# Performance work log

Measured on AMD Instinct MI355X. Metric: run time of the kernel, lower is better.

The kernel has to match this reference:

```python
import math
import jax, jax.numpy as jnp
import numpy as np

L, F, K = 3, 128, 20          # layers, hidden size, rbf size
CUTOFF = 5.0
B, NPER, EPER = 4, 4096, 49152  # graphs, nodes/graph, edges/graph
NVOC = 119                    # len(ase.data.atomic_numbers)
PNAMES = ['atom_emb','pot_W','pot_b','init_W1','init_b1','init_W2','init_b2','vec_w',
          'filt_W','filt_b','msg_W1','msg_b1','msg_W2','msg_b2','U_W','V_W',
          'upd_W1','upd_b1','upd_W2','upd_b2']


def _painn(atom_xyz, cell, nodes, atom_edges, edges_displacement, V_flat, E_flat, p):
    N = B * NPER
    pos = atom_xyz.reshape(N, 3)
    # edge_offset = cumsum(num_nodes) ; all graphs have NPER nodes
    off = (jnp.arange(B, dtype=atom_edges.dtype) * NPER)[:, None, None]
    edges = (atom_edges + off).reshape(B * EPER, 2)
    # calc_distance with periodic cell offsets
    disp = jnp.einsum('bec,bcd->bed', edges_displacement, cell).reshape(B * EPER, 3)
    send, recv = edges[:, 0], edges[:, 1]
    diff = pos[recv] - (pos[send] + disp)                       # [E,3]
    dist = jnp.sqrt(jnp.sum(diff * diff, axis=1, keepdims=True))  # [E,1]
    # sinc RBF expansion
    n_range = jnp.arange(1, K + 1, dtype=jnp.float32)
    edge_state = jnp.sin(dist * n_range * (math.pi / CUTOFF)) / dist  # [E,K]
    # init scalar features: Embedding(Z) || Linear(V) -> MLP
    s_atom = p['atom_emb'][nodes.reshape(N)]                    # [N,F]
    s_pot = V_flat @ p['pot_W'].T + p['pot_b']                  # [N,F]
    h = jnp.concatenate([s_atom, s_pot], axis=-1)
    s = jax.nn.silu(h @ p['init_W1'].T + p['init_b1']) @ p['init_W2'].T + p['init_b2']  # [N,F]
    # init vector features: no-bias Linear(1->F) on E field
    v = E_flat[:, :, None] * p['vec_w']                         # [N,3,F]
    cut = jnp.where(dist < CUTOFF, 0.5 * (jnp.cos(math.pi * dist / CUTOFF) + 1.0), 0.0)  # [E,1]
    dirn = diff / jnp.maximum(dist, 1e-12)                      # [E,3]
    s_list, v_list = [], []
    for l in range(L):
        # --- PaiNNInteraction ---
        fw = (edge_state @ p['filt_W'][l].T + p['filt_b'][l]) * cut                # [E,3F]
        so = jax.nn.silu(s @ p['msg_W1'][l].T + p['msg_b1'][l]) @ p['msg_W2'][l].T + p['msg_b2'][l]  # [N,3F]
        fo = fw * so[send]                                                          # [E,3F]
        g_sv, g_ev, g_ns = jnp.split(fo, 3, axis=1)
        msg_s = s[send] * g_ns                                                      # [E,F]
        msg_v = v[send] * g_sv[:, None, :] + g_ev[:, None, :] * dirn[:, :, None]    # [E,3,F]
        s = s + jax.ops.segment_sum(msg_s, recv, num_segments=N)
        v = v + jax.ops.segment_sum(msg_v, recv, num_segments=N)
        # --- PaiNNUpdate ---
        Uv = v @ p['U_W'][l].T                                                      # [N,3,F]
        Vv = v @ p['V_W'][l].T                                                      # [N,3,F]
        Vn = jnp.sqrt(jnp.sum(Vv * Vv, axis=1))                                     # [N,F]
        m = jnp.concatenate([s, Vn], axis=1)
        m = jax.nn.silu(m @ p['upd_W1'][l].T + p['upd_b1'][l]) @ p['upd_W2'][l].T + p['upd_b2'][l]
        a_ss, a_sv, a_vv = jnp.split(m, 3, axis=1)
        s = s + a_ss + a_sv * jnp.sum(Uv * Vv, axis=1)
        v = v + a_vv[:, None, :] * Uv
        s_list.append(s)
        v_list.append(v)
    # pack trajectory: [L,N,1,F] scalar || [L,N,3,F] vector -> [L,N,4,F]
    return jnp.concatenate([jnp.stack(s_list)[:, :, None, :], jnp.stack(v_list)], axis=2)


def setup_inputs() -> dict:
    key = jax.random.key(0)
    ks = iter(jax.random.split(key, 48))
    def nrm(shape, scale=0.05):
        return jax.random.normal(next(ks), shape, dtype=jnp.float32) * scale
    atom_xyz = jax.random.uniform(next(ks), (B, NPER, 3), dtype=jnp.float32) * 30.0
    cell = jnp.tile(jnp.eye(3, dtype=jnp.float32)[None] * 30.0, (B, 1, 1))
    nodes = jax.random.randint(next(ks), (B, NPER), 0, NVOC)
    e0 = jax.random.randint(next(ks), (B, EPER), 0, NPER)
    delta = jax.random.randint(next(ks), (B, EPER), 1, NPER)
    e1 = (e0 + delta) % NPER  # sender != receiver -> no zero-distance edges
    atom_edges = jnp.stack([e0, e1], axis=-1)
    edges_displacement = jax.random.randint(next(ks), (B, EPER, 3), -1, 2).astype(jnp.float32)
    V_flat = nrm((B * NPER, 1), 1.0)
    E_flat = nrm((B * NPER, 3), 1.0)
    params = dict(
        atom_emb=nrm((NVOC, F), 1.0),
        pot_W=nrm((F, 1)), pot_b=nrm((F,)),
        init_W1=nrm((F, 2 * F)), init_b1=nrm((F,)),
        init_W2=nrm((F, F)), init_b2=nrm((F,)),
        vec_w=nrm((F,)),
        filt_W=nrm((L, 3 * F, K)), filt_b=nrm((L, 3 * F)),
        msg_W1=nrm((L, F, F)), msg_b1=nrm((L, F)),
        msg_W2=nrm((L, 3 * F, F)), msg_b2=nrm((L, 3 * F)),
        U_W=nrm((L, F, F)), V_W=nrm((L, F, F)),
        upd_W1=nrm((L, F, 2 * F)), upd_b1=nrm((L, F)),
        upd_W2=nrm((L, 3 * F, F)), upd_b2=nrm((L, 3 * F)),
    )
    return dict(atom_xyz=atom_xyz, cell=cell, nodes=nodes, atom_edges=atom_edges,
                edges_displacement=edges_displacement, V_flat=V_flat, E_flat=E_flat, **params)


def reference(atom_xyz, cell, nodes, atom_edges, edges_displacement, V_flat, E_flat,
              atom_emb, pot_W, pot_b, init_W1, init_b1, init_W2, init_b2, vec_w,
              filt_W, filt_b, msg_W1, msg_b1, msg_W2, msg_b2, U_W, V_W,
              upd_W1, upd_b1, upd_W2, upd_b2):
    p = dict(zip(PNAMES, (atom_emb, pot_W, pot_b, init_W1, init_b1, init_W2, init_b2, vec_w,
                          filt_W, filt_b, msg_W1, msg_b1, msg_W2, msg_b2, U_W, V_W,
                          upd_W1, upd_b1, upd_W2, upd_b2)))
    return _painn(atom_xyz, cell, nodes, atom_edges, edges_displacement, V_flat, E_flat, p)
```

## Files before the change

kernel.cpp:

```cpp
#include <hip/hip_runtime.h>
#include <math.h>

#define NPER  4096
#define NTOT  16384
#define EPER  49152
#define ETOT  196608
#define FD    128
#define F3    384
#define KR    20
#define PI_F  3.14159265358979f

typedef unsigned short u16;
typedef __attribute__((ext_vector_type(8))) short s16x8;
typedef __attribute__((ext_vector_type(4))) float f32x4;
typedef _Float16 h16x2 __attribute__((ext_vector_type(2)));
typedef _Float16 h16x4 __attribute__((ext_vector_type(4)));
typedef _Float16 h16x8 __attribute__((ext_vector_type(8)));

#if defined(__has_builtin)
#if __has_builtin(__builtin_amdgcn_fdot2)
#define FDOT2(a,b,c) __builtin_amdgcn_fdot2((a),(b),(c),false)
#endif
#endif
#ifndef FDOT2
#define FDOT2(a,b,c) ((float)(a)[0]*(float)(b)[0] + (float)(a)[1]*(float)(b)[1] + (c))
#endif

__device__ __forceinline__ float silu_f(float x){ return x / (1.0f + __expf(-x)); }
__device__ __forceinline__ u16 f2b(float x){
    unsigned u = __float_as_uint(x);
    u = u + 0x7FFFu + ((u >> 16) & 1u);
    return (u16)(u >> 16);
}
__device__ __forceinline__ float b2f(u16 h){ return __uint_as_float(((unsigned)h) << 16); }

struct __align__(16) EdgeRec {
    float4 ed;
    h16x8  es0;
    h16x8  es1;
    h16x4  es2;
    h16x4  pad;
};

__global__ __launch_bounds__(256) void edge_kernel(
    const float* __restrict__ xyz, const float* __restrict__ cell,
    const int* __restrict__ aedges, const float* __restrict__ edisp,
    int* __restrict__ sendb, int* __restrict__ recvb,
    EdgeRec* __restrict__ erec, int* __restrict__ counts)
{
    int e = blockIdx.x * blockDim.x + threadIdx.x;
    if (e >= ETOT) return;
    int b = e / EPER;
    int s = aedges[(size_t)e*2+0] + b*NPER;
    int r = aedges[(size_t)e*2+1] + b*NPER;
    const float* cb = cell + b*9;
    float c0 = edisp[(size_t)e*3+0], c1 = edisp[(size_t)e*3+1], c2 = edisp[(size_t)e*3+2];
    float diff[3];
    #pragma unroll
    for (int d=0; d<3; ++d) {
        float disp = c0*cb[d] + c1*cb[3+d] + c2*cb[6+d];
        diff[d] = xyz[(size_t)r*3+d] - (xyz[(size_t)s*3+d] + disp);
    }
    float dist = sqrtf(diff[0]*diff[0]+diff[1]*diff[1]+diff[2]*diff[2]);
    float cut = (dist < 5.0f) ? 0.5f*(__cosf(PI_F*dist*0.2f)+1.0f) : 0.0f;
    float invg = 1.0f/fmaxf(dist,1e-12f);
    EdgeRec rec;
    rec.ed = make_float4(diff[0]*invg, diff[1]*invg, diff[2]*invg, cut);
    float theta = dist*(PI_F*0.2f);
    float s1 = __sinf(theta), cth = __cosf(theta);
    float scale = cut / dist;
    float twoc = 2.f*cth;
    float sm1 = 0.f, sk = s1;
    _Float16 esv[20];
    #pragma unroll
    for (int k=0;k<20;++k){
        esv[k] = (_Float16)(sk*scale);
        float nx = twoc*sk - sm1;
        sm1 = sk; sk = nx;
    }
    union { h16x8 v; _Float16 h[8]; } u0, u1;
    union { h16x4 v; _Float16 h[4]; } u2;
    #pragma unroll
    for (int i=0;i<8;++i){ u0.h[i]=esv[i]; u1.h[i]=esv[8+i]; }
    #pragma unroll
    for (int i=0;i<4;++i) u2.h[i]=esv[16+i];
    rec.es0=u0.v; rec.es1=u1.v; rec.es2=u2.v;
    rec.pad = (h16x4)((_Float16)0);
    erec[e] = rec;
    sendb[e]=s; recvb[e]=r;
    atomicAdd(&counts[r],1);
}

__global__ __launch_bounds__(1024) void scan_kernel(const int* __restrict__ counts,
                                                    int* __restrict__ row_off)
{
    __shared__ int sdata[1024];
    int t = threadIdx.x;
    int base = t * 16;
    int local[16];
    int s = 0;
    #pragma unroll
    for (int i=0;i<16;++i){ local[i]=s; s += counts[base+i]; }
    sdata[t] = s;
    __syncthreads();
    for (int off=1; off<1024; off<<=1) {
        int val = (t>=off) ? sdata[t-off] : 0;
        __syncthreads();
        sdata[t] += val;
        __syncthreads();
    }
    int chunk_off = (t==0) ? 0 : sdata[t-1];
    #pragma unroll
    for (int i=0;i<16;++i) row_off[base+i] = chunk_off + local[i];
    if (t==1023) row_off[NTOT] = sdata[1023];
}

__global__ __launch_bounds__(256) void fill_kernel(
    const int* __restrict__ recvb, const int* __restrict__ sendb,
    const EdgeRec* __restrict__ erec,
    const int* __restrict__ row_off, int* __restrict__ cursor,
    int* __restrict__ sd_csr, EdgeRec* __restrict__ erec_csr)
{
    int e = blockIdx.x * blockDim.x + threadIdx.x;
    if (e >= ETOT) return;
    int r = recvb[e];
    int slot = atomicAdd(&cursor[r], 1);
    int pos = row_off[r] + slot;
    sd_csr[pos] = sendb[e];
    erec_csr[pos] = erec[e];
}

__global__ __launch_bounds__(256) void wconv_kernel(
    const float* __restrict__ w0, const float* __restrict__ w1,
    const float* __restrict__ w2, const float* __restrict__ w3,
    const float* __restrict__ w4, const float* __restrict__ w5,
    const float* __restrict__ w6, const float* __restrict__ w7,
    u16* __restrict__ dst)
{
    int t = blockIdx.x*256 + threadIdx.x;
    if (t >= 589824) return;
    const float* src; int off; int d = t;
    if      (t < 32768)  { src=w0; off=t; }
    else if (t < 49152)  { src=w1; off=t-32768; }
    else if (t < 98304)  { src=w2; off=t-49152; }
    else if (t < 245760) { src=w3; off=t-98304; }
    else if (t < 294912) { int o=t-245760; int l=o>>14; int r=o&16383; src=w4; off=o;
                           d = 245760 + l*32768 + r; }
    else if (t < 344064) { int o=t-294912; int l=o>>14; int r=o&16383; src=w5; off=o;
                           d = 245760 + l*32768 + 16384 + r; }
    else if (t < 442368) { src=w6; off=t-344064; }
    else                 { src=w7; off=t-442368; }
    dst[d] = f2b(src[off]);
}

__global__ __launch_bounds__(256) void wfilt_kernel(const float* __restrict__ fW,
                                                    _Float16* __restrict__ dst)
{
    int t = blockIdx.x*256 + threadIdx.x;
    if (t < 3*F3*KR) dst[t] = (_Float16)fW[t];
}

__global__ __launch_bounds__(256) void hbuild_kernel(const int* __restrict__ nodes,
    const float* __restrict__ atom_emb, const float* __restrict__ V_flat,
    const float* __restrict__ pot_W, const float* __restrict__ pot_b,
    u16* __restrict__ h)
{
    int t = blockIdx.x * blockDim.x + threadIdx.x;
    int n = t >> 8, k = t & 255;
    float val;
    if (k < FD) val = atom_emb[(size_t)nodes[n]*FD + k];
    else { int f = k - FD; val = V_flat[n]*pot_W[f] + pot_b[f]; }
    h[t] = f2b(val);
}

__global__ __launch_bounds__(256) void v0_kernel(const float* __restrict__ E_flat,
    const float* __restrict__ vec_w, float* __restrict__ v0, u16* __restrict__ vq)
{
    int t = blockIdx.x * blockDim.x + threadIdx.x;
    int n = t / F3, r = t - n*F3;
    int c = r >> 7, f = r & 127;
    float val = E_flat[(size_t)n*3 + c] * vec_w[f];
    v0[t] = val;
    vq[((size_t)n*FD + f)*4 + c] = f2b(val);
}

template<int ACT>
__global__ __launch_bounds__(256) void bgemm_kernel(
    const u16* __restrict__ A, int lda,
    const u16* __restrict__ W, int Kdim,
    const float* __restrict__ bias,
    float* __restrict__ C, int ldc,
    u16* __restrict__ Cb, int ldcb,
    u16* __restrict__ Cq, int qoff)
{
    const int tid  = threadIdx.x;
    const int wave = tid >> 6, lane = tid & 63;
    const int q = lane >> 4, im = lane & 15;
    const int row0 = blockIdx.y*64 + wave*16;
    const int col0 = blockIdx.x*64;
    f32x4 acc[4];
    #pragma unroll
    for (int n=0;n<4;++n) acc[n] = (f32x4){0.f,0.f,0.f,0.f};
    const u16* Ap = A + (size_t)(row0+im)*lda + q*8;
    const u16* Wp = W + (size_t)(col0+im)*Kdim + q*8;
    for (int k0 = 0; k0 < Kdim; k0 += 32) {
        s16x8 af = *(const s16x8*)(Ap + k0);
        #pragma unroll
        for (int n=0;n<4;++n) {
            s16x8 bf = *(const s16x8*)(Wp + (size_t)n*16*Kdim + k0);
            acc[n] = __builtin_amdgcn_mfma_f32_16x16x32_bf16(af, bf, acc[n], 0, 0, 0);
        }
    }
    #pragma unroll
    for (int n=0;n<4;++n) {
        int col = col0 + n*16 + im;
        float bv = bias ? bias[col] : 0.f;
        #pragma unroll
        for (int r=0;r<4;++r) {
            int row = row0 + q*4 + r;
            float v = acc[n][r] + bv;
            if (ACT) v = silu_f(v);
            if (C)  C[(size_t)row*ldc + col] = v;
            if (Cb) Cb[(size_t)row*ldcb + col] = f2b(v);
            if (Cq) Cq[((size_t)row*FD + (col & 127))*4 + (col >> 7) + qoff] = f2b(v);
        }
    }
}

#define HID_OFF(row, col2b) ((unsigned)((row)*256 + (col2b)*2) ^ ((unsigned)((row)&7) << 4))

__global__ __launch_bounds__(512) void msgmlp_kernel(
    const u16* __restrict__ A,
    const u16* __restrict__ W1,
    const float* __restrict__ b1,
    const u16* __restrict__ W2,
    const float* __restrict__ b2,
    u16* __restrict__ sq)
{
    __shared__ u16 hid[64*FD];
    const int tid = threadIdx.x;
    const int wave = tid >> 6, lane = tid & 63;
    const int q = lane >> 4, im = lane & 15;
    const int rw = (wave >> 1) * 16;
    const int ch = wave & 1;
    const int row0 = blockIdx.x * 64;
    {
        f32x4 acc[4];
        #pragma unroll
        for (int n=0;n<4;++n) acc[n] = (f32x4){0.f,0.f,0.f,0.f};
        const u16* Ap = A + (size_t)(row0+rw+im)*FD + q*8;
        #pragma unroll
        for (int k0=0;k0<FD;k0+=32) {
            s16x8 af = *(const s16x8*)(Ap + k0);
            #pragma unroll
            for (int n=0;n<4;++n) {
                s16x8 bf = *(const s16x8*)(W1 + (size_t)(ch*64+n*16+im)*FD + k0 + q*8);
                acc[n] = __builtin_amdgcn_mfma_f32_16x16x32_bf16(af, bf, acc[n], 0, 0, 0);
            }
        }
        #pragma unroll
        for (int n=0;n<4;++n) {
            int col = ch*64 + n*16 + im;
            float bv = b1[col];
            #pragma unroll
            for (int r=0;r<4;++r) {
                int row = rw + q*4 + r;
                *(u16*)((char*)hid + HID_OFF(row, col)) = f2b(silu_f(acc[n][r]+bv));
            }
        }
    }
    __syncthreads();
    s16x8 af[4];
    {
        int row = rw + im;
        #pragma unroll
        for (int k=0;k<4;++k)
            af[k] = *(const s16x8*)((char*)hid + HID_OFF(row, k*32+q*8));
    }
    #pragma unroll
    for (int jj=0;jj<4;++jj) {
        int j = ch*4 + jj;
        f32x4 a2[3];
        #pragma unroll
        for (int g=0;g<3;++g) a2[g] = (f32x4){0.f,0.f,0.f,0.f};
        #pragma unroll
        for (int k=0;k<4;++k) {
            #pragma unroll
            for (int g=0;g<3;++g) {
                s16x8 bf = *(const s16x8*)(W2 + (size_t)(g*128 + j*16 + im)*FD + k*32 + q*8);
                a2[g] = __builtin_amdgcn_mfma_f32_16x16x32_bf16(af[k], bf, a2[g], 0, 0, 0);
            }
        }
        int fcol = j*16 + im;
        float c0 = b2[fcol], c1 = b2[FD+fcol], c2 = b2[2*FD+fcol];
        #pragma unroll
        for (int r=0;r<4;++r) {
            int row = row0 + rw + q*4 + r;
            size_t t4 = ((size_t)row*FD + fcol)*4;
            unsigned pk = (unsigned)f2b(a2[0][r]+c0) | ((unsigned)f2b(a2[1][r]+c1) << 16);
            *(unsigned*)(sq + t4) = pk;
            sq[t4+2] = f2b(a2[2][r]+c2);
        }
    }
}

__global__ __launch_bounds__(512) void updmlp_kernel(
    const u16* __restrict__ A,
    const u16* __restrict__ W1,
    const float* __restrict__ b1,
    const u16* __restrict__ W2,
    const float* __restrict__ b2,
    const float* __restrict__ s_mid, const float* __restrict__ dotb,
    const float* __restrict__ v_mid, const float* __restrict__ Uv,
    float* __restrict__ outp, u16* __restrict__ s_bf,
    u16* __restrict__ sq, u16* __restrict__ vq)
{
    __shared__ u16 hid[64*FD];
    const int tid = threadIdx.x;
    const int wave = tid >> 6, lane = tid & 63;
    const int q = lane >> 4, im = lane & 15;
    const int rw = (wave >> 1) * 16;
    const int ch = wave & 1;
    const int row0 = blockIdx.x * 64;
    {
        f32x4 acc[4];
        #pragma unroll
        for (int n=0;n<4;++n) acc[n] = (f32x4){0.f,0.f,0.f,0.f};
        const u16* Ap = A + (size_t)(row0+rw+im)*256 + q*8;
        #pragma unroll
        for (int k0=0;k0<256;k0+=32) {
            s16x8 af = *(const s16x8*)(Ap + k0);
            #pragma unroll
            for (int n=0;n<4;++n) {
                s16x8 bf = *(const s16x8*)(W1 + (size_t)(ch*64+n*16+im)*256 + k0 + q*8);
                acc[n] = __builtin_amdgcn_mfma_f32_16x16x32_bf16(af, bf, acc[n], 0, 0, 0);
            }
        }
        #pragma unroll
        for (int n=0;n<4;++n) {
            int col = ch*64 + n*16 + im;
            float bv = b1[col];
            #pragma unroll
            for (int r=0;r<4;++r) {
                int row = rw + q*4 + r;
                *(u16*)((char*)hid + HID_OFF(row, col)) = f2b(silu_f(acc[n][r]+bv));
            }
        }
    }
    __syncthreads();
    s16x8 af[4];
    {
        int row = rw + im;
        #pragma unroll
        for (int k=0;k<4;++k)
            af[k] = *(const s16x8*)((char*)hid + HID_OFF(row, k*32+q*8));
    }
    #pragma unroll
    for (int jj=0;jj<4;++jj) {
        int j = ch*4 + jj;
        f32x4 a2[3];
        #pragma unroll
        for (int g=0;g<3;++g) a2[g] = (f32x4){0.f,0.f,0.f,0.f};
        #pragma unroll
        for (int k=0;k<4;++k) {
            #pragma unroll
            for (int g=0;g<3;++g) {
                s16x8 bf = *(const s16x8*)(W2 + (size_t)(g*128 + j*16 + im)*FD + k*32 + q*8);
                a2[g] = __builtin_amdgcn_mfma_f32_16x16x32_bf16(af[k], bf, a2[g], 0, 0, 0);
            }
        }
        int fcol = j*16 + im;
        float b_ss = b2[fcol], b_sv = b2[FD+fcol], b_vv = b2[2*FD+fcol];
        #pragma unroll
        for (int r=0;r<4;++r) {
            int row = row0 + rw + q*4 + r;
            float a_ss = a2[0][r] + b_ss;
            float a_sv = a2[1][r] + b_sv;
            float a_vv = a2[2][r] + b_vv;
            size_t t = (size_t)row*FD + fcol;
            float sval = s_mid[t] + a_ss + a_sv*dotb[t];
            outp[(size_t)row*512 + fcol] = sval;
            s_bf[t] = f2b(sval);
            sq[t*4 + 3] = f2b(sval);
            ushort4 pack;
            #pragma unroll
            for (int c=0;c<3;++c) {
                size_t vi = ((size_t)row*3 + c)*FD + fcol;
                float vval = v_mid[vi] + a_vv*Uv[((size_t)row*4 + c)*FD + fcol];
                outp[(size_t)row*512 + (1+c)*FD + fcol] = vval;
                ((u16*)&pack)[c] = f2b(vval);
            }
            ((u16*)&pack)[3] = 0;
            *(ushort4*)(vq + t*4) = pack;
        }
    }
}

__global__ __launch_bounds__(256) void uvdot_kernel(
    const u16* __restrict__ A,
    const u16* __restrict__ W,
    float* __restrict__ Uv,
    float* __restrict__ dotb,
    u16* __restrict__ mbuf)
{
    const int tid  = threadIdx.x;
    const int wave = tid >> 6, lane = tid & 63;
    const int q = lane >> 4, im = lane & 15;
    const int row0 = blockIdx.x*64 + wave*16;
    const int node = (row0 >> 2) + q;
    const u16* Ap = A + (size_t)(row0+im)*FD + q*8;
    s16x8 af[4];
    #pragma unroll
    for (int k=0;k<4;++k) af[k] = *(const s16x8*)(Ap + k*32);
    #pragma unroll
    for (int j=0;j<8;++j) {
        f32x4 aU = (f32x4){0.f,0.f,0.f,0.f};
        f32x4 aV = (f32x4){0.f,0.f,0.f,0.f};
        const u16* WpU = W + (size_t)(j*16+im)*FD + q*8;
        const u16* WpV = WpU + (size_t)128*FD;
        #pragma unroll
        for (int k=0;k<4;++k) {
            s16x8 bU = *(const s16x8*)(WpU + k*32);
            s16x8 bV = *(const s16x8*)(WpV + k*32);
            aU = __builtin_amdgcn_mfma_f32_16x16x32_bf16(af[k], bU, aU, 0, 0, 0);
            aV = __builtin_amdgcn_mfma_f32_16x16x32_bf16(af[k], bV, aV, 0, 0, 0);
        }
        int fcol = j*16 + im;
        float u0=aU[0], u1=aU[1], u2=aU[2];
        float w0=aV[0], w1=aV[1], w2=aV[2];
        dotb[(size_t)node*FD + fcol] = u0*w0 + u1*w1 + u2*w2;
        mbuf[(size_t)node*256 + FD + fcol] = f2b(sqrtf(w0*w0 + w1*w1 + w2*w2));
        size_t ub = ((size_t)node*4)*FD + fcol;
        Uv[ub]      = u0;
        Uv[ub+FD]   = u1;
        Uv[ub+2*FD] = u2;
    }
}

__device__ __forceinline__ void edge_step(
    const EdgeRec& er, ushort4 s4, ushort4 v4,
    const h16x2* wp,
    float b0, float b1, float b2,
    float& acc_s, float& av0, float& av1, float& av2)
{
    union { h16x8 v; h16x2 p[4]; } e0, e1;
    union { h16x4 v; h16x2 p[2]; } e2;
    e0.v = er.es0; e1.v = er.es1; e2.v = er.es2;
    h16x2 ep[10] = {e0.p[0],e0.p[1],e0.p[2],e0.p[3],
                    e1.p[0],e1.p[1],e1.p[2],e1.p[3],
                    e2.p[0],e2.p[1]};
    float4 ed = er.ed;
    float d0=0.f, d1=0.f, d2=0.f;
    #pragma unroll
    for (int j=0;j<10;++j){
        d0 = FDOT2(ep[j], wp[j],    d0);
        d1 = FDOT2(ep[j], wp[10+j], d1);
        d2 = FDOT2(ep[j], wp[20+j], d2);
    }
    float g_sv = d0 + b0*ed.w;
    float g_ev = d1 + b1*ed.w;
    float g_ns = d2 + b2*ed.w;
    float fo_sv = g_sv * b2f(s4.x);
    float fo_ev = g_ev * b2f(s4.y);
    float fo_ns = g_ns * b2f(s4.z);
    acc_s += b2f(s4.w) * fo_ns;
    av0 += b2f(v4.x)*fo_sv + fo_ev*ed.x;
    av1 += b2f(v4.y)*fo_sv + fo_ev*ed.y;
    av2 += b2f(v4.z)*fo_sv + fo_ev*ed.z;
}

__global__ __launch_bounds__(256) __attribute__((amdgpu_waves_per_eu(4,8)))
void agg_kernel(
    const float* __restrict__ s_prev_f, int s_ldaf,
    const float* __restrict__ v_prev_f, int v_nstrf,
    const ushort4* __restrict__ sq, const ushort4* __restrict__ vq,
    const EdgeRec* __restrict__ erec_csr,
    const int* __restrict__ sd_csr, const int* __restrict__ row_off,
    const _Float16* __restrict__ wf, const float* __restrict__ fb,
    float* __restrict__ s_mid, float* __restrict__ v_mid,
    u16* __restrict__ vmid4_bf, u16* __restrict__ mbuf)
{
    const int f   = threadIdx.x & 127;
    const int sub = threadIdx.x >> 7;
    h16x2 wp[30];
    #pragma unroll
    for (int rsel=0; rsel<3; ++rsel){
        const h16x4* rp = (const h16x4*)(wf + (size_t)(rsel*FD + f)*KR);
        #pragma unroll
        for (int i=0;i<5;++i){
            union { h16x4 v; h16x2 p[2]; } t; t.v = rp[i];
            wp[rsel*10+2*i]   = t.p[0];
            wp[rsel*10+2*i+1] = t.p[1];
        }
    }
    const float b0 = fb[f], b1 = fb[FD+f], b2 = fb[2*FD+f];

    const int n = blockIdx.x*2 + sub;
    const int beg = __builtin_amdgcn_readfirstlane(row_off[n]);
    const int end = __builtin_amdgcn_readfirstlane(row_off[n+1]);
    float acc_s=0.f, av0=0.f, av1=0.f, av2=0.f;

    int i0 = (beg   < end) ? beg   : 0;
    int i1 = (beg+1 < end) ? beg+1 : i0;
    int sd0 = __builtin_amdgcn_readfirstlane(sd_csr[i0]);
    int sd1 = __builtin_amdgcn_readfirstlane(sd_csr[i1]);
    ushort4 sA = sq[(size_t)sd0*FD + f];
    ushort4 vA = vq[(size_t)sd0*FD + f];
    ushort4 sB = sq[(size_t)sd1*FD + f];
    ushort4 vB = vq[(size_t)sd1*FD + f];
    EdgeRec r0 = erec_csr[i0];
    EdgeRec r1 = erec_csr[i1];

    for (int idx = beg; idx + 2 <= end; idx += 2) {
        int j0 = (idx+2 < end) ? idx+2 : 0;
        int j1 = (idx+3 < end) ? idx+3 : j0;
        int nsd0 = __builtin_amdgcn_readfirstlane(sd_csr[j0]);
        int nsd1 = __builtin_amdgcn_readfirstlane(sd_csr[j1]);
        ushort4 nsA = sq[(size_t)nsd0*FD + f];
        ushort4 nvA = vq[(size_t)nsd0*FD + f];
        ushort4 nsB = sq[(size_t)nsd1*FD + f];
        ushort4 nvB = vq[(size_t)nsd1*FD + f];
        EdgeRec nr0 = erec_csr[j0];
        EdgeRec nr1 = erec_csr[j1];

        edge_step(r0, sA, vA, wp, b0,b1,b2, acc_s, av0, av1, av2);
        edge_step(r1, sB, vB, wp, b0,b1,b2, acc_s, av0, av1, av2);

        sA=nsA; vA=nvA; sB=nsB; vB=nvB; r0=nr0; r1=nr1;
    }
    if (((end - beg) & 1) && beg < end) {
        edge_step(r0, sA, vA, wp, b0,b1,b2, acc_s, av0, av1, av2);
    }

    float smv = s_prev_f[(size_t)n*s_ldaf+f] + acc_s;
    s_mid[(size_t)n*FD+f] = smv;
    mbuf[(size_t)n*256+f] = f2b(smv);
    const float* vp = v_prev_f + (size_t)n*v_nstrf;
    float o0 = vp[f]+av0, o1 = vp[FD+f]+av1, o2 = vp[2*FD+f]+av2;
    size_t vo = (size_t)n*F3;
    v_mid[vo+f]=o0;        v_mid[vo+FD+f]=o1;        v_mid[vo+2*FD+f]=o2;
    size_t v4 = (size_t)n*512;
    vmid4_bf[v4+f]=f2b(o0); vmid4_bf[v4+FD+f]=f2b(o1); vmid4_bf[v4+2*FD+f]=f2b(o2);
}

extern "C" void kernel_launch(void* const* d_in, const int* in_sizes, int n_in,
                              void* d_out, int out_size, void* d_ws, size_t ws_size,
                              hipStream_t stream)
{
    (void)in_sizes; (void)n_in; (void)out_size; (void)ws_size;
    const float* atom_xyz = (const float*)d_in[0];
    const float* cell     = (const float*)d_in[1];
    const int*   nodes    = (const int*)d_in[2];
    const int*   aedges   = (const int*)d_in[3];
    const float* edisp    = (const float*)d_in[4];
    const float* V_flat   = (const float*)d_in[5];
    const float* E_flat   = (const float*)d_in[6];
    const float* atom_emb = (const float*)d_in[7];
    const float* pot_W    = (const float*)d_in[8];
    const float* pot_b    = (const float*)d_in[9];
    const float* init_W1  = (const float*)d_in[10];
    const float* init_b1  = (const float*)d_in[11];
    const float* init_W2  = (const float*)d_in[12];
    const float* init_b2  = (const float*)d_in[13];
    const float* vec_w    = (const float*)d_in[14];
    const float* filt_W   = (const float*)d_in[15];
    const float* filt_b   = (const float*)d_in[16];
    const float* msg_W1   = (const float*)d_in[17];
    const float* msg_b1   = (const float*)d_in[18];
    const float* msg_W2   = (const float*)d_in[19];
    const float* msg_b2   = (const float*)d_in[20];
    const float* U_W      = (const float*)d_in[21];
    const float* V_W      = (const float*)d_in[22];
    const float* upd_W1   = (const float*)d_in[23];
    const float* upd_b1   = (const float*)d_in[24];
    const float* upd_W2   = (const float*)d_in[25];
    const float* upd_b2   = (const float*)d_in[26];

    float* out = (float*)d_out;
    char* base = (char*)d_ws;
    size_t o = 0;
    auto alloc = [&](size_t bytes)->char* { char* r = base + o; o += (bytes + 255) & ~(size_t)255; return r; };

    float* s0     = (float*)alloc((size_t)NTOT*FD*4);
    float* v0     = (float*)alloc((size_t)NTOT*F3*4);
    float* s_mid  = (float*)alloc((size_t)NTOT*FD*4);
    float* v_mid  = (float*)alloc((size_t)NTOT*F3*4);
    float* Uv4    = (float*)alloc((size_t)NTOT*4*FD*4);
    float* dotb   = (float*)alloc((size_t)NTOT*FD*4);
    EdgeRec* erec     = (EdgeRec*)alloc((size_t)ETOT*sizeof(EdgeRec));
    EdgeRec* erec_csr = (EdgeRec*)alloc((size_t)ETOT*sizeof(EdgeRec));
    u16* h_bf     = (u16*)alloc((size_t)NTOT*256*2);
    u16* s_bf     = (u16*)alloc((size_t)NTOT*FD*2);
    u16* sq       = (u16*)alloc((size_t)NTOT*FD*4*2);
    u16* vq       = (u16*)alloc((size_t)NTOT*FD*4*2);
    u16* hid_bf   = (u16*)alloc((size_t)NTOT*FD*2);
    u16* vmid4_bf = (u16*)alloc((size_t)NTOT*4*FD*2);
    u16* wts      = (u16*)alloc((size_t)589824*2);
    _Float16* wf16 = (_Float16*)alloc((size_t)3*F3*KR*2);
    int* sendb    = (int*)alloc((size_t)ETOT*4);
    int* recvb    = (int*)alloc((size_t)ETOT*4);
    int* sd_csr   = (int*)alloc((size_t)ETOT*4);
    int* row_off  = (int*)alloc((size_t)(NTOT+1)*4);
    int* counts   = (int*)alloc((size_t)NTOT*4);
    int* cursor   = (int*)alloc((size_t)NTOT*4);

    hipMemsetAsync(counts, 0, NTOT*sizeof(int), stream);
    hipMemsetAsync(cursor, 0, NTOT*sizeof(int), stream);
    hipMemsetAsync(vmid4_bf, 0, (size_t)NTOT*4*FD*2, stream);

    edge_kernel<<<ETOT/256, 256, 0, stream>>>(atom_xyz, cell, aedges, edisp,
        sendb, recvb, erec, counts);
    scan_kernel<<<1, 1024, 0, stream>>>(counts, row_off);
    fill_kernel<<<ETOT/256, 256, 0, stream>>>(recvb, sendb, erec,
        row_off, cursor, sd_csr, erec_csr);
    wconv_kernel<<<(589824+255)/256, 256, 0, stream>>>(
        init_W1, init_W2, msg_W1, msg_W2, U_W, V_W, upd_W1, upd_W2, wts);
    wfilt_kernel<<<(3*F3*KR+255)/256, 256, 0, stream>>>(filt_W, wf16);

    const u16* w_init1 = wts + 0;
    const u16* w_init2 = wts + 32768;
    const u16* w_msg1  = wts + 49152;
    const u16* w_msg2  = wts + 98304;
    const u16* w_UV    = wts + 245760;
    const u16* w_upd1  = wts + 344064;
    const u16* w_upd2  = wts + 442368;

    hbuild_kernel<<<NTOT*256/256, 256, 0, stream>>>(nodes, atom_emb, V_flat, pot_W, pot_b, h_bf);
    bgemm_kernel<1><<<dim3(FD/64, NTOT/64), 256, 0, stream>>>(
        h_bf, 256, w_init1, 256, init_b1, (float*)nullptr, 0, hid_bf, FD, (u16*)nullptr, 0);
    bgemm_kernel<0><<<dim3(FD/64, NTOT/64), 256, 0, stream>>>(
        hid_bf, FD, w_init2, FD, init_b2, s0, FD, s_bf, FD, sq, 3);
    v0_kernel<<<NTOT*F3/256, 256, 0, stream>>>(E_flat, vec_w, v0, vq);

    const float* s_prev_f = s0;  int s_ldaf  = FD;
    const float* v_prev_f = v0;  int v_nstrf = 3*FD;
    for (int l = 0; l < 3; ++l) {
        msgmlp_kernel<<<NTOT/64, 512, 0, stream>>>(
            s_bf, w_msg1 + (size_t)l*16384, msg_b1 + (size_t)l*FD,
            w_msg2 + (size_t)l*49152, msg_b2 + (size_t)l*F3, sq);
        agg_kernel<<<NTOT/2, 256, 0, stream>>>(s_prev_f, s_ldaf, v_prev_f, v_nstrf,
            (const ushort4*)sq, (const ushort4*)vq, erec_csr, sd_csr, row_off,
            wf16 + (size_t)l*F3*KR, filt_b + (size_t)l*F3, s_mid, v_mid, vmid4_bf, h_bf);
        uvdot_kernel<<<NTOT*4/64, 256, 0, stream>>>(
            vmid4_bf, w_UV + (size_t)l*32768, Uv4, dotb, h_bf);
        float* outp = out + (size_t)l*NTOT*512;
        updmlp_kernel<<<NTOT/64, 512, 0, stream>>>(
            h_bf, w_upd1 + (size_t)l*32768, upd_b1 + (size_t)l*FD,
            w_upd2 + (size_t)l*49152, upd_b2 + (size_t)l*F3,
            s_mid, dotb, v_mid, Uv4, outp, s_bf, sq, vq);
        s_prev_f = outp;        s_ldaf  = 512;
        v_prev_f = outp + FD;   v_nstrf = 512;
    }
}
```

Before: 769.6 us.

## Shrink message and update MLP tiles to 16 rows with 4 waves per block

```diff
diff --git a/kernel.cpp b/kernel.cpp
--- a/kernel.cpp
+++ b/kernel.cpp
@@ -229,7 +229,7 @@
 
 #define HID_OFF(row, col2b) ((unsigned)((row)*256 + (col2b)*2) ^ ((unsigned)((row)&7) << 4))
 
-__global__ __launch_bounds__(512) void msgmlp_kernel(
+__global__ __launch_bounds__(256) void msgmlp_kernel(
     const u16* __restrict__ A,
     const u16* __restrict__ W1,
     const float* __restrict__ b1,
@@ -237,49 +237,44 @@
     const float* __restrict__ b2,
     u16* __restrict__ sq)
 {
-    __shared__ u16 hid[64*FD];
+    __shared__ u16 hid[16*FD];
     const int tid = threadIdx.x;
     const int wave = tid >> 6, lane = tid & 63;
     const int q = lane >> 4, im = lane & 15;
-    const int rw = (wave >> 1) * 16;
-    const int ch = wave & 1;
-    const int row0 = blockIdx.x * 64;
+    const int row0 = blockIdx.x * 16;
     {
-        f32x4 acc[4];
-        #pragma unroll
-        for (int n=0;n<4;++n) acc[n] = (f32x4){0.f,0.f,0.f,0.f};
-        const u16* Ap = A + (size_t)(row0+rw+im)*FD + q*8;
+        f32x4 acc[2];
+        #pragma unroll
+        for (int n=0;n<2;++n) acc[n] = (f32x4){0.f,0.f,0.f,0.f};
+        const u16* Ap = A + (size_t)(row0+im)*FD + q*8;
         #pragma unroll
         for (int k0=0;k0<FD;k0+=32) {
             s16x8 af = *(const s16x8*)(Ap + k0);
             #pragma unroll
-            for (int n=0;n<4;++n) {
-                s16x8 bf = *(const s16x8*)(W1 + (size_t)(ch*64+n*16+im)*FD + k0 + q*8);
+            for (int n=0;n<2;++n) {
+                s16x8 bf = *(const s16x8*)(W1 + (size_t)(wave*32+n*16+im)*FD + k0 + q*8);
                 acc[n] = __builtin_amdgcn_mfma_f32_16x16x32_bf16(af, bf, acc[n], 0, 0, 0);
             }
         }
         #pragma unroll
-        for (int n=0;n<4;++n) {
-            int col = ch*64 + n*16 + im;
+        for (int n=0;n<2;++n) {
+            int col = wave*32 + n*16 + im;
             float bv = b1[col];
             #pragma unroll
             for (int r=0;r<4;++r) {
-                int row = rw + q*4 + r;
+                int row = q*4 + r;
                 *(u16*)((char*)hid + HID_OFF(row, col)) = f2b(silu_f(acc[n][r]+bv));
             }
         }
     }
     __syncthreads();
     s16x8 af[4];
-    {
-        int row = rw + im;
-        #pragma unroll
-        for (int k=0;k<4;++k)
-            af[k] = *(const s16x8*)((char*)hid + HID_OFF(row, k*32+q*8));
-    }
-    #pragma unroll
-    for (int jj=0;jj<4;++jj) {
-        int j = ch*4 + jj;
+    #pragma unroll
+    for (int k=0;k<4;++k)
+        af[k] = *(const s16x8*)((char*)hid + HID_OFF(im, k*32+q*8));
+    #pragma unroll
+    for (int jj=0;jj<2;++jj) {
+        int j = wave*2 + jj;
         f32x4 a2[3];
         #pragma unroll
         for (int g=0;g<3;++g) a2[g] = (f32x4){0.f,0.f,0.f,0.f};
@@ -295,7 +290,7 @@
         float c0 = b2[fcol], c1 = b2[FD+fcol], c2 = b2[2*FD+fcol];
         #pragma unroll
         for (int r=0;r<4;++r) {
-            int row = row0 + rw + q*4 + r;
+            int row = row0 + q*4 + r;
             size_t t4 = ((size_t)row*FD + fcol)*4;
             unsigned pk = (unsigned)f2b(a2[0][r]+c0) | ((unsigned)f2b(a2[1][r]+c1) << 16);
             *(unsigned*)(sq + t4) = pk;
@@ -304,7 +299,7 @@
     }
 }
 
-__global__ __launch_bounds__(512) void updmlp_kernel(
+__global__ __launch_bounds__(256) void updmlp_kernel(
     const u16* __restrict__ A,
     const u16* __restrict__ W1,
     const float* __restrict__ b1,
@@ -315,49 +310,44 @@
     float* __restrict__ outp, u16* __restrict__ s_bf,
     u16* __restrict__ sq, u16* __restrict__ vq)
 {
-    __shared__ u16 hid[64*FD];
+    __shared__ u16 hid[16*FD];
     const int tid = threadIdx.x;
     const int wave = tid >> 6, lane = tid & 63;
     const int q = lane >> 4, im = lane & 15;
-    const int rw = (wave >> 1) * 16;
-    const int ch = wave & 1;
-    const int row0 = blockIdx.x * 64;
+    const int row0 = blockIdx.x * 16;
     {
-        f32x4 acc[4];
-        #pragma unroll
-        for (int n=0;n<4;++n) acc[n] = (f32x4){0.f,0.f,0.f,0.f};
-        const u16* Ap = A + (size_t)(row0+rw+im)*256 + q*8;
+        f32x4 acc[2];
+        #pragma unroll
+        for (int n=0;n<2;++n) acc[n] = (f32x4){0.f,0.f,0.f,0.f};
+        const u16* Ap = A + (size_t)(row0+im)*256 + q*8;
         #pragma unroll
         for (int k0=0;k0<256;k0+=32) {
             s16x8 af = *(const s16x8*)(Ap + k0);
             #pragma unroll
-            for (int n=0;n<4;++n) {
-                s16x8 bf = *(const s16x8*)(W1 + (size_t)(ch*64+n*16+im)*256 + k0 + q*8);
+            for (int n=0;n<2;++n) {
+                s16x8 bf = *(const s16x8*)(W1 + (size_t)(wave*32+n*16+im)*256 + k0 + q*8);
                 acc[n] = __builtin_amdgcn_mfma_f32_16x16x32_bf16(af, bf, acc[n], 0, 0, 0);
             }
         }
         #pragma unroll
-        for (int n=0;n<4;++n) {
-            int col = ch*64 + n*16 + im;
+        for (int n=0;n<2;++n) {
+            int col = wave*32 + n*16 + im;
             float bv = b1[col];
             #pragma unroll
             for (int r=0;r<4;++r) {
-                int row = rw + q*4 + r;
+                int row = q*4 + r;
                 *(u16*)((char*)hid + HID_OFF(row, col)) = f2b(silu_f(acc[n][r]+bv));
             }
         }
     }
     __syncthreads();
     s16x8 af[4];
-    {
-        int row = rw + im;
-        #pragma unroll
-        for (int k=0;k<4;++k)
-            af[k] = *(const s16x8*)((char*)hid + HID_OFF(row, k*32+q*8));
-    }
-    #pragma unroll
-    for (int jj=0;jj<4;++jj) {
-        int j = ch*4 + jj;
+    #pragma unroll
+    for (int k=0;k<4;++k)
+        af[k] = *(const s16x8*)((char*)hid + HID_OFF(im, k*32+q*8));
+    #pragma unroll
+    for (int jj=0;jj<2;++jj) {
+        int j = wave*2 + jj;
         f32x4 a2[3];
         #pragma unroll
         for (int g=0;g<3;++g) a2[g] = (f32x4){0.f,0.f,0.f,0.f};
@@ -373,7 +363,7 @@
         float b_ss = b2[fcol], b_sv = b2[FD+fcol], b_vv = b2[2*FD+fcol];
         #pragma unroll
         for (int r=0;r<4;++r) {
-            int row = row0 + rw + q*4 + r;
+            int row = row0 + q*4 + r;
             float a_ss = a2[0][r] + b_ss;
             float a_sv = a2[1][r] + b_sv;
             float a_vv = a2[2][r] + b_vv;
@@ -635,7 +625,7 @@
     const float* s_prev_f = s0;  int s_ldaf  = FD;
     const float* v_prev_f = v0;  int v_nstrf = 3*FD;
     for (int l = 0; l < 3; ++l) {
-        msgmlp_kernel<<<NTOT/64, 512, 0, stream>>>(
+        msgmlp_kernel<<<NTOT/16, 256, 0, stream>>>(
             s_bf, w_msg1 + (size_t)l*16384, msg_b1 + (size_t)l*FD,
             w_msg2 + (size_t)l*49152, msg_b2 + (size_t)l*F3, sq);
         agg_kernel<<<NTOT/2, 256, 0, stream>>>(s_prev_f, s_ldaf, v_prev_f, v_nstrf,
@@ -644,7 +634,7 @@
         uvdot_kernel<<<NTOT*4/64, 256, 0, stream>>>(
             vmid4_bf, w_UV + (size_t)l*32768, Uv4, dotb, h_bf);
         float* outp = out + (size_t)l*NTOT*512;
-        updmlp_kernel<<<NTOT/64, 512, 0, stream>>>(
+        updmlp_kernel<<<NTOT/16, 256, 0, stream>>>(
             h_bf, w_upd1 + (size_t)l*32768, upd_b1 + (size_t)l*FD,
             w_upd2 + (size_t)l*49152, upd_b2 + (size_t)l*F3,
             s_mid, dotb, v_mid, Uv4, outp, s_bf, sq, vq);
```

Measured after the change: 711.5 us. -7.6%, faster.
